# Kernel optimization log

Measured on AMD Instinct MI355X. Metric: run time of the kernel, lower is better.

The kernel has to match this reference:

```python
import jax, jax.numpy as jnp
import numpy as np

B, C, H, Wd = 4, 64, 64, 64


def setup_inputs() -> dict:
    key = jax.random.key(0)
    k1, k2, k3 = jax.random.split(key, 3)
    x = jax.random.normal(k1, (B, C, H, Wd), dtype=jnp.float32)
    W = jax.random.normal(k2, (C, C), dtype=jnp.float32) * (1.0 / np.sqrt(C))
    b = jax.random.normal(k3, (C,), dtype=jnp.float32) * 0.01
    return {"x": x, "W": W, "b": b}


def reference(x, W, b):
    Bz, Cz, Hz, Wz = x.shape
    N = Hz * Wz
    xf = x.reshape(Bz, Cz, N)                      # values [B,C,N]
    # shared 1x1 conv for queries and keys (same module instance in torch)
    qk = jnp.einsum('oc,bcn->bon', W, xf) + b[None, :, None]  # [B,C,N]
    # scores[b,n,m] = sum_c q[b,c,n] * k[b,c,m], scaled by 1/N
    scores = jnp.einsum('bcn,bcm->bnm', qk, qk) / N           # [B,N,N]
    attn = jax.nn.softmax(scores, axis=-1)                    # softmax over m
    # out[b,c,n] = sum_m values[b,c,m] * attn[b,n,m]
    out = jnp.einsum('bcm,bnm->bcn', xf, attn)
    return out.reshape(Bz, Cz, Hz, Wz)
```

## Files before the change

### kernel.cpp

```cpp
#include <hip/hip_runtime.h>
#include <hip/hip_bf16.h>

#define BATCH 4
#define NSP   4096

#define QKSCALE 0.0187675376f

typedef __bf16 bf16x8v __attribute__((ext_vector_type(8)));
typedef __bf16 bf16x4v __attribute__((ext_vector_type(4)));
typedef short  shortx4 __attribute__((ext_vector_type(4)));
typedef float  floatx4 __attribute__((ext_vector_type(4)));

static __device__ __forceinline__ shortx4 bf4_bits(bf16x4v v) {
    union { bf16x4v b; shortx4 s; } u; u.b = v; return u.s;
}

static __device__ __forceinline__ float fast_exp2(float x) {
#if __has_builtin(__builtin_amdgcn_exp2f)
    return __builtin_amdgcn_exp2f(x);
#else
    return exp2f(x);
#endif
}

static __device__ __forceinline__ floatx4 mfma_pv(shortx4 a, shortx4 b, floatx4 c) {
#if __has_builtin(__builtin_amdgcn_mfma_f32_16x16x16bf16_1k)
    return __builtin_amdgcn_mfma_f32_16x16x16bf16_1k(a, b, c, 0, 0, 0);
#else
    floatx4 d;
    asm("v_mfma_f32_16x16x16_bf16 %0, %1, %2, %3" : "=&v"(d) : "v"(a), "v"(b), "v"(c));
    return d;
#endif
}

__global__ __launch_bounds__(256) void qk_kernel(const float* __restrict__ x,
                                                 const float* __restrict__ Wm,
                                                 const float* __restrict__ bias,
                                                 __bf16* __restrict__ qkT,
                                                 __bf16* __restrict__ xbf) {
    __shared__ __align__(16) __bf16 xT[64 * 72];

    const int t  = threadIdx.x;
    const int b  = blockIdx.x >> 6;
    const int n0 = (blockIdx.x & 63) << 6;

#pragma unroll
    for (int p = 0; p < 4; ++p) {
        const int c  = p * 16 + (t >> 4);
        const int n4 = (t & 15) * 4;
        const float4 v = *(const float4*)(x + (size_t)(b * 64 + c) * 4096 + n0 + n4);
        xT[(n4 + 0) * 72 + c] = (__bf16)(v.x * QKSCALE);
        xT[(n4 + 1) * 72 + c] = (__bf16)(v.y * QKSCALE);
        xT[(n4 + 2) * 72 + c] = (__bf16)(v.z * QKSCALE);
        xT[(n4 + 3) * 72 + c] = (__bf16)(v.w * QKSCALE);
        bf16x4v xv;
        xv[0] = (__bf16)v.x; xv[1] = (__bf16)v.y; xv[2] = (__bf16)v.z; xv[3] = (__bf16)v.w;
        *(bf16x4v*)(xbf + (size_t)(b * 64 + c) * 4096 + n0 + n4) = xv;
    }
    __syncthreads();

    const int w = t >> 6, lane = t & 63, quad = lane >> 4, l16 = lane & 15;
    const bf16x8v a0 = *(const bf16x8v*)(xT + (w * 16 + l16) * 72 + quad * 8);
    const bf16x8v a1 = *(const bf16x8v*)(xT + (w * 16 + l16) * 72 + 32 + quad * 8);

    floatx4 acc[4];
#pragma unroll
    for (int ot = 0; ot < 4; ++ot) {
        const float* wr = Wm + (ot * 16 + l16) * 64;
        float4 wa = *(const float4*)(wr + quad * 8);
        float4 wb = *(const float4*)(wr + quad * 8 + 4);
        float4 wc = *(const float4*)(wr + 32 + quad * 8);
        float4 wd = *(const float4*)(wr + 32 + quad * 8 + 4);
        bf16x8v b0, b1;
        b0[0]=(__bf16)wa.x; b0[1]=(__bf16)wa.y; b0[2]=(__bf16)wa.z; b0[3]=(__bf16)wa.w;
        b0[4]=(__bf16)wb.x; b0[5]=(__bf16)wb.y; b0[6]=(__bf16)wb.z; b0[7]=(__bf16)wb.w;
        b1[0]=(__bf16)wc.x; b1[1]=(__bf16)wc.y; b1[2]=(__bf16)wc.z; b1[3]=(__bf16)wc.w;
        b1[4]=(__bf16)wd.x; b1[5]=(__bf16)wd.y; b1[6]=(__bf16)wd.z; b1[7]=(__bf16)wd.w;
        acc[ot] = floatx4{0.f, 0.f, 0.f, 0.f};
        acc[ot] = __builtin_amdgcn_mfma_f32_16x16x32_bf16(a0, b0, acc[ot], 0, 0, 0);
        acc[ot] = __builtin_amdgcn_mfma_f32_16x16x32_bf16(a1, b1, acc[ot], 0, 0, 0);
    }
    __syncthreads();

#pragma unroll
    for (int ot = 0; ot < 4; ++ot) {
        const float bo = bias[ot * 16 + l16] * QKSCALE;
#pragma unroll
        for (int r = 0; r < 4; ++r)
            xT[(w * 16 + quad * 4 + r) * 72 + ot * 16 + l16] = (__bf16)(acc[ot][r] + bo);
    }
    __syncthreads();

    const int n = t >> 2, seg = t & 3;
    __bf16* dst = qkT + (size_t)(b * 4096 + n0 + n) * 64 + seg * 16;
    *(bf16x8v*)dst       = *(const bf16x8v*)(xT + n * 72 + seg * 16);
    *(bf16x8v*)(dst + 8) = *(const bf16x8v*)(xT + n * 72 + seg * 16 + 8);
}

template<int SPLIT, int ITERS>
__global__ __launch_bounds__(256, 4) void attn_kernel(const __bf16* __restrict__ xbf,
                                                      const __bf16* __restrict__ qkT,
                                                      __bf16* __restrict__ Opart,
                                                      float* __restrict__ Lpart) {
    __shared__ __align__(16) char smem[36864];
    __bf16* Klds = (__bf16*)smem;
    __bf16* Vlds = (__bf16*)(smem + 18432);
    float*  Olds = (float*)smem;

    const int t   = threadIdx.x;
    const int blk = blockIdx.x;
    const int xcd = blk & 7;
    const int b   = xcd >> 1;
    const int sub = ((blk >> 3) << 1) | (xcd & 1);
    const int qt  = sub / SPLIT;
    const int s   = sub % SPLIT;
    const int n0  = qt << 7;
    const int pblk = (b * 32 + qt) * SPLIT + s;

    const int w = t >> 6, lane = t & 63, quad = lane >> 4, l16 = lane & 15;

    const __bf16* kgl = qkT + (size_t)b * 4096 * 64;
    const __bf16* vgl = xbf + (size_t)b * 64 * 4096;

    bf16x8v fq[2][2];
#pragma unroll
    for (int qt2 = 0; qt2 < 2; ++qt2) {
        const __bf16* qrow = kgl + (size_t)(n0 + w * 32 + qt2 * 16 + l16) * 64;
        fq[qt2][0] = *(const bf16x8v*)(qrow + quad * 8);
        fq[qt2][1] = *(const bf16x8v*)(qrow + 32 + quad * 8);
    }

    floatx4 oacc[2][4];
#pragma unroll
    for (int i = 0; i < 2; ++i)
#pragma unroll
        for (int j = 0; j < 4; ++j) oacc[i][j] = floatx4{0.f, 0.f, 0.f, 0.f};
    float rs[2] = {0.f, 0.f};

    const int srow = t >> 3;
    const int sg   = (t & 7) * 8;
    uint4 kst0, kst1, vst0, vst1;
    auto stage_load = [&](int m0) {
        kst0 = *(const uint4*)(kgl + (size_t)(m0 + srow) * 64 + sg);
        kst1 = *(const uint4*)(kgl + (size_t)(m0 + srow + 32) * 64 + sg);
        vst0 = *(const uint4*)(vgl + (size_t)srow * 4096 + m0 + sg);
        vst1 = *(const uint4*)(vgl + (size_t)(srow + 32) * 4096 + m0 + sg);
    };
    auto stage_write = [&](int buf) {
        __bf16* kd = Klds + buf * 4608;
        __bf16* vd = Vlds + buf * 4608;
        *(uint4*)(kd + srow * 72 + sg)        = kst0;
        *(uint4*)(kd + (srow + 32) * 72 + sg) = kst1;
        *(uint4*)(vd + srow * 72 + sg)        = vst0;
        *(uint4*)(vd + (srow + 32) * 72 + sg) = vst1;
    };

    const int mbase = s * (64 * ITERS);
    stage_load(mbase);
    stage_write(0);
    int cur = 0;

    for (int it = 0; it < ITERS; ++it) {
        const int m0 = mbase + (it << 6);
        if (it + 1 < ITERS) stage_load(m0 + 64);
        __syncthreads();
        const __bf16* Kc = Klds + cur * 4608;
        const __bf16* Vc = Vlds + cur * 4608;

#pragma unroll
        for (int mt = 0; mt < 4; ++mt) {
            const __bf16* kr = Kc + (mt * 16 + l16) * 72;
            bf16x8v ak0 = *(const bf16x8v*)(kr + quad * 8);
            bf16x8v ak1 = *(const bf16x8v*)(kr + 32 + quad * 8);
            shortx4 pk[2];
#pragma unroll
            for (int qt2 = 0; qt2 < 2; ++qt2) {
                floatx4 sT = {0.f, 0.f, 0.f, 0.f};
                sT = __builtin_amdgcn_mfma_f32_16x16x32_bf16(ak0, fq[qt2][0], sT, 0, 0, 0);
                sT = __builtin_amdgcn_mfma_f32_16x16x32_bf16(ak1, fq[qt2][1], sT, 0, 0, 0);
                float p0 = fast_exp2(sT[0]), p1 = fast_exp2(sT[1]);
                float p2 = fast_exp2(sT[2]), p3 = fast_exp2(sT[3]);
                rs[qt2] += (p0 + p1) + (p2 + p3);
                bf16x4v pv;
                pv[0] = (__bf16)p0; pv[1] = (__bf16)p1; pv[2] = (__bf16)p2; pv[3] = (__bf16)p3;
                pk[qt2] = bf4_bits(pv);
            }
#pragma unroll
            for (int ct = 0; ct < 4; ++ct) {
                shortx4 av = *(const shortx4*)(Vc + (ct * 16 + l16) * 72 + mt * 16 + quad * 4);
                oacc[0][ct] = mfma_pv(av, pk[0], oacc[0][ct]);
                oacc[1][ct] = mfma_pv(av, pk[1], oacc[1][ct]);
            }
        }

        if (it + 1 < ITERS) stage_write(cur ^ 1);
        cur ^= 1;
    }

#pragma unroll
    for (int qt2 = 0; qt2 < 2; ++qt2) {
        float v = rs[qt2];
        v += __shfl_xor(v, 16, 64);
        v += __shfl_xor(v, 32, 64);
        if (quad == 0)
            Lpart[(size_t)pblk * 128 + w * 32 + qt2 * 16 + l16] = v;
    }

    __syncthreads();

#pragma unroll
    for (int qt2 = 0; qt2 < 2; ++qt2)
#pragma unroll
        for (int ct = 0; ct < 4; ++ct)
#pragma unroll
            for (int r = 0; r < 4; ++r)
                Olds[(ct * 16 + quad * 4 + r) * 132 + w * 32 + qt2 * 16 + l16] = oacc[qt2][ct][r];
    __syncthreads();

    const int c = t >> 2, seg = t & 3;
#pragma unroll
    for (int i = 0; i < 4; ++i) {
        floatx4 v0 = *(const floatx4*)(Olds + c * 132 + seg * 32 + i * 8);
        floatx4 v1 = *(const floatx4*)(Olds + c * 132 + seg * 32 + i * 8 + 4);
        bf16x8v pk;
        pk[0]=(__bf16)v0[0]; pk[1]=(__bf16)v0[1]; pk[2]=(__bf16)v0[2]; pk[3]=(__bf16)v0[3];
        pk[4]=(__bf16)v1[0]; pk[5]=(__bf16)v1[1]; pk[6]=(__bf16)v1[2]; pk[7]=(__bf16)v1[3];
        *(bf16x8v*)(Opart + (size_t)pblk * 8192 + c * 128 + seg * 32 + i * 8) = pk;
    }
}

template<int SPLIT>
__global__ __launch_bounds__(256) void reduce_kernel(const __bf16* __restrict__ Opart,
                                                     const float* __restrict__ Lpart,
                                                     float* __restrict__ out) {
    const int blk = blockIdx.x;
    const int bq = blk >> 2, cq = blk & 3;
    const int b = bq >> 5, qt = bq & 31;
    const int t = threadIdx.x;
    const int c  = cq * 16 + (t >> 4);
    const int q8 = (t & 15) * 8;

    float l[8] = {0.f,0.f,0.f,0.f,0.f,0.f,0.f,0.f};
#pragma unroll
    for (int s = 0; s < SPLIT; ++s) {
        const float* lp = Lpart + ((size_t)bq * SPLIT + s) * 128 + q8;
        float4 u = *(const float4*)lp;
        float4 v = *(const float4*)(lp + 4);
        l[0]+=u.x; l[1]+=u.y; l[2]+=u.z; l[3]+=u.w;
        l[4]+=v.x; l[5]+=v.y; l[6]+=v.z; l[7]+=v.w;
    }
    float a[8] = {0.f,0.f,0.f,0.f,0.f,0.f,0.f,0.f};
#pragma unroll
    for (int s = 0; s < SPLIT; ++s) {
        bf16x8v v = *(const bf16x8v*)(Opart + ((size_t)bq * SPLIT + s) * 8192 + c * 128 + q8);
#pragma unroll
        for (int k = 0; k < 8; ++k) a[k] += (float)v[k];
    }
    float* op = out + (size_t)(b * 64 + c) * 4096 + qt * 128 + q8;
    float4 o0, o1;
    o0.x = a[0]/l[0]; o0.y = a[1]/l[1]; o0.z = a[2]/l[2]; o0.w = a[3]/l[3];
    o1.x = a[4]/l[4]; o1.y = a[5]/l[5]; o1.z = a[6]/l[6]; o1.w = a[7]/l[7];
    *(float4*)op       = o0;
    *(float4*)(op + 4) = o1;
}

extern "C" void kernel_launch(void* const* d_in, const int* in_sizes, int n_in,
                              void* d_out, int out_size, void* d_ws, size_t ws_size,
                              hipStream_t stream) {
    const float* x    = (const float*)d_in[0];
    const float* Wm   = (const float*)d_in[1];
    const float* bias = (const float*)d_in[2];
    float* out = (float*)d_out;

    char* ws = (char*)d_ws;
    __bf16* qkT = (__bf16*)ws;
    __bf16* xbf = (__bf16*)(ws + 2097152);

    qk_kernel<<<BATCH * (NSP / 64), 256, 0, stream>>>(x, Wm, bias, qkT, xbf);

    const size_t HEAD = 2097152 + 2097152;
    const size_t needBig = HEAD + (size_t)1024 * 8192 * 2 + (size_t)1024 * 128 * 4;
    if (ws_size >= needBig) {
        __bf16* Opart = (__bf16*)(ws + HEAD);
        float*  Lpart = (float*)(ws + HEAD + (size_t)1024 * 8192 * 2);
        attn_kernel<8, 8><<<BATCH * 32 * 8, 256, 0, stream>>>(xbf, qkT, Opart, Lpart);
        reduce_kernel<8><<<512, 256, 0, stream>>>(Opart, Lpart, out);
    } else {
        __bf16* Opart = (__bf16*)(ws + HEAD);
        float*  Lpart = (float*)(ws + HEAD + (size_t)512 * 8192 * 2);
        attn_kernel<4, 16><<<BATCH * 32 * 4, 256, 0, stream>>>(xbf, qkT, Opart, Lpart);
        reduce_kernel<4><<<512, 256, 0, stream>>>(Opart, Lpart, out);
    }
}
```

Measured before the change: 97.27 us.

## Switch attention to 32x32x16 MFMA with 256-query tiles and permlane swap

Measured after the change: 102.6 us. 5.5% more time.

```diff
diff --git a/kernel.cpp b/kernel.cpp
--- a/kernel.cpp
+++ b/kernel.cpp
@@ -8,12 +8,9 @@
 
 typedef __bf16 bf16x8v __attribute__((ext_vector_type(8)));
 typedef __bf16 bf16x4v __attribute__((ext_vector_type(4)));
-typedef short  shortx4 __attribute__((ext_vector_type(4)));
 typedef float  floatx4 __attribute__((ext_vector_type(4)));
-
-static __device__ __forceinline__ shortx4 bf4_bits(bf16x4v v) {
-    union { bf16x4v b; shortx4 s; } u; u.b = v; return u.s;
-}
+typedef float  floatx16 __attribute__((ext_vector_type(16)));
+typedef unsigned uivec2 __attribute__((ext_vector_type(2)));
 
 static __device__ __forceinline__ float fast_exp2(float x) {
 #if __has_builtin(__builtin_amdgcn_exp2f)
@@ -23,13 +20,18 @@
 #endif
 }
 
-static __device__ __forceinline__ floatx4 mfma_pv(shortx4 a, shortx4 b, floatx4 c) {
-#if __has_builtin(__builtin_amdgcn_mfma_f32_16x16x16bf16_1k)
-    return __builtin_amdgcn_mfma_f32_16x16x16bf16_1k(a, b, c, 0, 0, 0);
+static __device__ __forceinline__ unsigned pkbf(float a, float b) {
+    union { __bf16 h[2]; unsigned u; } x;
+    x.h[0] = (__bf16)a; x.h[1] = (__bf16)b;
+    return x.u;
+}
+
+static __device__ __forceinline__ void plswap(unsigned &a, unsigned &b) {
+#if __has_builtin(__builtin_amdgcn_permlane32_swap)
+    uivec2 r = __builtin_amdgcn_permlane32_swap(a, b, false, false);
+    a = r[0]; b = r[1];
 #else
-    floatx4 d;
-    asm("v_mfma_f32_16x16x16_bf16 %0, %1, %2, %3" : "=&v"(d) : "v"(a), "v"(b), "v"(c));
-    return d;
+    asm("v_permlane32_swap_b32 %0, %1" : "+v"(a), "+v"(b));
 #endif
 }
 
@@ -98,13 +100,12 @@
 }
 
 template<int SPLIT, int ITERS>
-__global__ __launch_bounds__(256, 4) void attn_kernel(const __bf16* __restrict__ xbf,
+__global__ __launch_bounds__(256, 2) void attn_kernel(const __bf16* __restrict__ xbf,
                                                       const __bf16* __restrict__ qkT,
                                                       __bf16* __restrict__ Opart,
                                                       float* __restrict__ Lpart) {
-    __shared__ __align__(16) char smem[36864];
-    __bf16* Klds = (__bf16*)smem;
-    __bf16* Vlds = (__bf16*)(smem + 18432);
+    __shared__ __align__(16) char smem[66560];
+    __bf16* Vlds = (__bf16*)smem;
     float*  Olds = (float*)smem;
 
     const int t   = threadIdx.x;
@@ -114,45 +115,38 @@
     const int sub = ((blk >> 3) << 1) | (xcd & 1);
     const int qt  = sub / SPLIT;
     const int s   = sub % SPLIT;
-    const int n0  = qt << 7;
-    const int pblk = (b * 32 + qt) * SPLIT + s;
-
-    const int w = t >> 6, lane = t & 63, quad = lane >> 4, l16 = lane & 15;
+    const int n0  = qt << 8;
+    const int pblk = (b * 16 + qt) * SPLIT + s;
+
+    const int w = t >> 6, lane = t & 63, l31 = lane & 31, hi = lane >> 5;
 
     const __bf16* kgl = qkT + (size_t)b * 4096 * 64;
     const __bf16* vgl = xbf + (size_t)b * 64 * 4096;
 
-    bf16x8v fq[2][2];
+    bf16x8v qf[2][4];
 #pragma unroll
     for (int qt2 = 0; qt2 < 2; ++qt2) {
-        const __bf16* qrow = kgl + (size_t)(n0 + w * 32 + qt2 * 16 + l16) * 64;
-        fq[qt2][0] = *(const bf16x8v*)(qrow + quad * 8);
-        fq[qt2][1] = *(const bf16x8v*)(qrow + 32 + quad * 8);
-    }
-
-    floatx4 oacc[2][4];
-#pragma unroll
-    for (int i = 0; i < 2; ++i)
-#pragma unroll
-        for (int j = 0; j < 4; ++j) oacc[i][j] = floatx4{0.f, 0.f, 0.f, 0.f};
+        const __bf16* qrow = kgl + (size_t)(n0 + w * 64 + qt2 * 32 + l31) * 64;
+#pragma unroll
+        for (int kb = 0; kb < 4; ++kb)
+            qf[qt2][kb] = *(const bf16x8v*)(qrow + kb * 16 + hi * 8);
+    }
+
+    floatx16 oacc[2][2] = {};
     float rs[2] = {0.f, 0.f};
 
-    const int srow = t >> 3;
-    const int sg   = (t & 7) * 8;
-    uint4 kst0, kst1, vst0, vst1;
+    const int c0    = t >> 3;
+    const int col8  = t & 7;
+    const int slot0 = ((col8 ^ (c0 & 7)) * 8);
+    uint4 vst0, vst1;
     auto stage_load = [&](int m0) {
-        kst0 = *(const uint4*)(kgl + (size_t)(m0 + srow) * 64 + sg);
-        kst1 = *(const uint4*)(kgl + (size_t)(m0 + srow + 32) * 64 + sg);
-        vst0 = *(const uint4*)(vgl + (size_t)srow * 4096 + m0 + sg);
-        vst1 = *(const uint4*)(vgl + (size_t)(srow + 32) * 4096 + m0 + sg);
+        vst0 = *(const uint4*)(vgl + (size_t)c0 * 4096 + m0 + col8 * 8);
+        vst1 = *(const uint4*)(vgl + (size_t)(c0 + 32) * 4096 + m0 + col8 * 8);
     };
     auto stage_write = [&](int buf) {
-        __bf16* kd = Klds + buf * 4608;
-        __bf16* vd = Vlds + buf * 4608;
-        *(uint4*)(kd + srow * 72 + sg)        = kst0;
-        *(uint4*)(kd + (srow + 32) * 72 + sg) = kst1;
-        *(uint4*)(vd + srow * 72 + sg)        = vst0;
-        *(uint4*)(vd + (srow + 32) * 72 + sg) = vst1;
+        __bf16* vd = Vlds + buf * 4096;
+        *(uint4*)(vd + c0 * 64 + slot0)        = vst0;
+        *(uint4*)(vd + (c0 + 32) * 64 + slot0) = vst1;
     };
 
     const int mbase = s * (64 * ITERS);
@@ -164,32 +158,55 @@
         const int m0 = mbase + (it << 6);
         if (it + 1 < ITERS) stage_load(m0 + 64);
         __syncthreads();
-        const __bf16* Kc = Klds + cur * 4608;
-        const __bf16* Vc = Vlds + cur * 4608;
-
-#pragma unroll
-        for (int mt = 0; mt < 4; ++mt) {
-            const __bf16* kr = Kc + (mt * 16 + l16) * 72;
-            bf16x8v ak0 = *(const bf16x8v*)(kr + quad * 8);
-            bf16x8v ak1 = *(const bf16x8v*)(kr + 32 + quad * 8);
-            shortx4 pk[2];
+        const __bf16* Vc = Vlds + cur * 4096;
+
+#pragma unroll
+        for (int mt = 0; mt < 2; ++mt) {
+            bf16x8v kf[4];
+#pragma unroll
+            for (int kb = 0; kb < 4; ++kb)
+                kf[kb] = *(const bf16x8v*)(kgl + (size_t)(m0 + mt * 32 + l31) * 64 + kb * 16 + hi * 8);
+
+            bf16x8v vf[2][2];
+#pragma unroll
+            for (int ct = 0; ct < 2; ++ct)
+#pragma unroll
+                for (int ks = 0; ks < 2; ++ks) {
+                    const int c  = ct * 32 + l31;
+                    const int sl = ((mt * 4 + ks * 2 + hi) ^ (c & 7)) * 8;
+                    vf[ct][ks] = *(const bf16x8v*)(Vc + c * 64 + sl);
+                }
+
 #pragma unroll
             for (int qt2 = 0; qt2 < 2; ++qt2) {
-                floatx4 sT = {0.f, 0.f, 0.f, 0.f};
-                sT = __builtin_amdgcn_mfma_f32_16x16x32_bf16(ak0, fq[qt2][0], sT, 0, 0, 0);
-                sT = __builtin_amdgcn_mfma_f32_16x16x32_bf16(ak1, fq[qt2][1], sT, 0, 0, 0);
-                float p0 = fast_exp2(sT[0]), p1 = fast_exp2(sT[1]);
-                float p2 = fast_exp2(sT[2]), p3 = fast_exp2(sT[3]);
-                rs[qt2] += (p0 + p1) + (p2 + p3);
-                bf16x4v pv;
-                pv[0] = (__bf16)p0; pv[1] = (__bf16)p1; pv[2] = (__bf16)p2; pv[3] = (__bf16)p3;
-                pk[qt2] = bf4_bits(pv);
-            }
-#pragma unroll
-            for (int ct = 0; ct < 4; ++ct) {
-                shortx4 av = *(const shortx4*)(Vc + (ct * 16 + l16) * 72 + mt * 16 + quad * 4);
-                oacc[0][ct] = mfma_pv(av, pk[0], oacc[0][ct]);
-                oacc[1][ct] = mfma_pv(av, pk[1], oacc[1][ct]);
+                floatx16 acc = {};
+#pragma unroll
+                for (int kb = 0; kb < 4; ++kb)
+                    acc = __builtin_amdgcn_mfma_f32_32x32x16_bf16(kf[kb], qf[qt2][kb], acc, 0, 0, 0);
+
+                float p[16];
+                float sum = 0.f;
+#pragma unroll
+                for (int i = 0; i < 16; ++i) { p[i] = fast_exp2(acc[i]); sum += p[i]; }
+                rs[qt2] += sum;
+
+                unsigned wd0 = pkbf(p[0],  p[1]),  wd1 = pkbf(p[2],  p[3]);
+                unsigned wd2 = pkbf(p[4],  p[5]),  wd3 = pkbf(p[6],  p[7]);
+                unsigned wd4 = pkbf(p[8],  p[9]),  wd5 = pkbf(p[10], p[11]);
+                unsigned wd6 = pkbf(p[12], p[13]), wd7 = pkbf(p[14], p[15]);
+                plswap(wd0, wd2);
+                plswap(wd1, wd3);
+                plswap(wd4, wd6);
+                plswap(wd5, wd7);
+                union { unsigned u[4]; bf16x8v v; } pb0, pb1;
+                pb0.u[0] = wd0; pb0.u[1] = wd1; pb0.u[2] = wd2; pb0.u[3] = wd3;
+                pb1.u[0] = wd4; pb1.u[1] = wd5; pb1.u[2] = wd6; pb1.u[3] = wd7;
+
+#pragma unroll
+                for (int ct = 0; ct < 2; ++ct) {
+                    oacc[qt2][ct] = __builtin_amdgcn_mfma_f32_32x32x16_bf16(vf[ct][0], pb0.v, oacc[qt2][ct], 0, 0, 0);
+                    oacc[qt2][ct] = __builtin_amdgcn_mfma_f32_32x32x16_bf16(vf[ct][1], pb1.v, oacc[qt2][ct], 0, 0, 0);
+                }
             }
         }
 
@@ -199,11 +216,9 @@
 
 #pragma unroll
     for (int qt2 = 0; qt2 < 2; ++qt2) {
-        float v = rs[qt2];
-        v += __shfl_xor(v, 16, 64);
-        v += __shfl_xor(v, 32, 64);
-        if (quad == 0)
-            Lpart[(size_t)pblk * 128 + w * 32 + qt2 * 16 + l16] = v;
+        float v = rs[qt2] + __shfl_xor(rs[qt2], 32, 64);
+        if (lane < 32)
+            Lpart[(size_t)pblk * 256 + w * 64 + qt2 * 32 + l31] = v;
     }
 
     __syncthreads();
@@ -211,21 +226,23 @@
 #pragma unroll
     for (int qt2 = 0; qt2 < 2; ++qt2)
 #pragma unroll
-        for (int ct = 0; ct < 4; ++ct)
-#pragma unroll
-            for (int r = 0; r < 4; ++r)
-                Olds[(ct * 16 + quad * 4 + r) * 132 + w * 32 + qt2 * 16 + l16] = oacc[qt2][ct][r];
-    __syncthreads();
-
-    const int c = t >> 2, seg = t & 3;
-#pragma unroll
-    for (int i = 0; i < 4; ++i) {
-        floatx4 v0 = *(const floatx4*)(Olds + c * 132 + seg * 32 + i * 8);
-        floatx4 v1 = *(const floatx4*)(Olds + c * 132 + seg * 32 + i * 8 + 4);
+        for (int ct = 0; ct < 2; ++ct)
+#pragma unroll
+            for (int r = 0; r < 16; ++r) {
+                const int c = ct * 32 + (r & 3) + 8 * (r >> 2) + 4 * hi;
+                Olds[c * 260 + w * 64 + qt2 * 32 + l31] = oacc[qt2][ct][r];
+            }
+    __syncthreads();
+
+    const int c = t >> 2, qb = (t & 3) * 64;
+#pragma unroll
+    for (int i = 0; i < 8; ++i) {
+        floatx4 v0 = *(const floatx4*)(Olds + c * 260 + qb + i * 8);
+        floatx4 v1 = *(const floatx4*)(Olds + c * 260 + qb + i * 8 + 4);
         bf16x8v pk;
         pk[0]=(__bf16)v0[0]; pk[1]=(__bf16)v0[1]; pk[2]=(__bf16)v0[2]; pk[3]=(__bf16)v0[3];
         pk[4]=(__bf16)v1[0]; pk[5]=(__bf16)v1[1]; pk[6]=(__bf16)v1[2]; pk[7]=(__bf16)v1[3];
-        *(bf16x8v*)(Opart + (size_t)pblk * 8192 + c * 128 + seg * 32 + i * 8) = pk;
+        *(bf16x8v*)(Opart + (size_t)pblk * 16384 + c * 256 + qb + i * 8) = pk;
     }
 }
 
@@ -234,16 +251,16 @@
                                                      const float* __restrict__ Lpart,
                                                      float* __restrict__ out) {
     const int blk = blockIdx.x;
-    const int bq = blk >> 2, cq = blk & 3;
-    const int b = bq >> 5, qt = bq & 31;
+    const int bq = blk >> 3, cq = blk & 7;
+    const int b = bq >> 4, qt = bq & 15;
     const int t = threadIdx.x;
-    const int c  = cq * 16 + (t >> 4);
-    const int q8 = (t & 15) * 8;
+    const int c  = cq * 8 + (t >> 5);
+    const int q8 = (t & 31) * 8;
 
     float l[8] = {0.f,0.f,0.f,0.f,0.f,0.f,0.f,0.f};
 #pragma unroll
     for (int s = 0; s < SPLIT; ++s) {
-        const float* lp = Lpart + ((size_t)bq * SPLIT + s) * 128 + q8;
+        const float* lp = Lpart + ((size_t)bq * SPLIT + s) * 256 + q8;
         float4 u = *(const float4*)lp;
         float4 v = *(const float4*)(lp + 4);
         l[0]+=u.x; l[1]+=u.y; l[2]+=u.z; l[3]+=u.w;
@@ -252,11 +269,11 @@
     float a[8] = {0.f,0.f,0.f,0.f,0.f,0.f,0.f,0.f};
 #pragma unroll
     for (int s = 0; s < SPLIT; ++s) {
-        bf16x8v v = *(const bf16x8v*)(Opart + ((size_t)bq * SPLIT + s) * 8192 + c * 128 + q8);
+        bf16x8v v = *(const bf16x8v*)(Opart + ((size_t)bq * SPLIT + s) * 16384 + c * 256 + q8);
 #pragma unroll
         for (int k = 0; k < 8; ++k) a[k] += (float)v[k];
     }
-    float* op = out + (size_t)(b * 64 + c) * 4096 + qt * 128 + q8;
+    float* op = out + (size_t)(b * 64 + c) * 4096 + qt * 256 + q8;
     float4 o0, o1;
     o0.x = a[0]/l[0]; o0.y = a[1]/l[1]; o0.z = a[2]/l[2]; o0.w = a[3]/l[3];
     o1.x = a[4]/l[4]; o1.y = a[5]/l[5]; o1.z = a[6]/l[6]; o1.w = a[7]/l[7];
@@ -279,16 +296,16 @@
     qk_kernel<<<BATCH * (NSP / 64), 256, 0, stream>>>(x, Wm, bias, qkT, xbf);
 
     const size_t HEAD = 2097152 + 2097152;
-    const size_t needBig = HEAD + (size_t)1024 * 8192 * 2 + (size_t)1024 * 128 * 4;
+    const size_t needBig = HEAD + (size_t)512 * 16384 * 2 + (size_t)512 * 256 * 4;
     if (ws_size >= needBig) {
         __bf16* Opart = (__bf16*)(ws + HEAD);
-        float*  Lpart = (float*)(ws + HEAD + (size_t)1024 * 8192 * 2);
-        attn_kernel<8, 8><<<BATCH * 32 * 8, 256, 0, stream>>>(xbf, qkT, Opart, Lpart);
+        float*  Lpart = (float*)(ws + HEAD + (size_t)512 * 16384 * 2);
+        attn_kernel<8, 8><<<BATCH * 16 * 8, 256, 0, stream>>>(xbf, qkT, Opart, Lpart);
         reduce_kernel<8><<<512, 256, 0, stream>>>(Opart, Lpart, out);
     } else {
         __bf16* Opart = (__bf16*)(ws + HEAD);
-        float*  Lpart = (float*)(ws + HEAD + (size_t)512 * 8192 * 2);
-        attn_kernel<4, 16><<<BATCH * 32 * 4, 256, 0, stream>>>(xbf, qkT, Opart, Lpart);
+        float*  Lpart = (float*)(ws + HEAD + (size_t)256 * 16384 * 2);
+        attn_kernel<4, 16><<<BATCH * 16 * 4, 256, 0, stream>>>(xbf, qkT, Opart, Lpart);
         reduce_kernel<4><<<512, 256, 0, stream>>>(Opart, Lpart, out);
     }
 }
```
